# Performance work log

Measured on AMD Instinct MI355X. Metric: run time of the kernel, lower is better.

The kernel has to match this reference:

```python
import jax, jax.numpy as jnp
import numpy as np

WIN = 12     # SAMv3 window_size
HEADS = 8    # num_heads

def _window(t, win=WIN):
    B, H, W, C = t.shape
    t = t.reshape(B, H // win, win, W // win, win, C).transpose(0, 1, 3, 2, 4, 5)
    return t.reshape(B, (H // win) * (W // win), win * win, C)

def _unwindow(t, H, W, win=WIN):
    B, nW, S, C = t.shape
    t = t.reshape(B, H // win, W // win, win, win, C).transpose(0, 1, 3, 2, 4, 5)
    return t.reshape(B, H, W, C)

def _sam(fq, fkv, bias, wq, wk, wv, wo, bo):
    # Windowed, masked cross-frame multi-head attention (SAMv3).
    # fq, fkv: (B, C, H, W); bias: (B, nW, 1, 1, S) additive mask bias.
    B, C, H, W = fq.shape
    hd = C // HEADS
    scale = hd ** -0.5
    q = _window(jnp.einsum('bchw,cd->bhwd', fq, wq))   # (B,nW,S,C)
    k = _window(jnp.einsum('bchw,cd->bhwd', fkv, wk))
    v = _window(jnp.einsum('bchw,cd->bhwd', fkv, wv))
    nW, S = q.shape[1], q.shape[2]
    q = q.reshape(B, nW, S, HEADS, hd)
    k = k.reshape(B, nW, S, HEADS, hd)
    v = v.reshape(B, nW, S, HEADS, hd)
    attn = jnp.einsum('bnqhd,bnkhd->bnhqk', q, k) * scale + bias
    attn = jax.nn.softmax(attn, axis=-1)
    out = jnp.einsum('bnhqk,bnkhd->bnqhd', attn, v).reshape(B, nW, S, C)
    out = out @ wo + bo
    return _unwindow(out, H, W).transpose(0, 3, 1, 2)  # (B, C, H, W)

def setup_inputs() -> dict:
    key = jax.random.key(0)
    B, C, T, H, W = 2, 384, 2, 192, 192
    ks = jax.random.split(key, 16)
    d = {}
    d['x'] = jax.random.normal(ks[0], (B, C, T, H, W), jnp.float32)
    d['mask'] = jax.random.randint(ks[1], (B, T, 1, H, W), 0, 2, jnp.int32)
    names = ['sam1_wq', 'sam1_wk', 'sam1_wv', 'sam1_wo',
             'sam2_wq', 'sam2_wk', 'sam2_wv', 'sam2_wo',
             'proj1_w', 'proj2_w']
    for i, n in enumerate(names):
        d[n] = jax.random.normal(ks[2 + i], (C, C), jnp.float32) * 0.02
    d['sam1_bo'] = jnp.zeros((C,), jnp.float32)
    d['sam2_bo'] = jnp.zeros((C,), jnp.float32)
    d['proj1_b'] = jnp.zeros((C,), jnp.float32)
    d['proj2_b'] = jnp.zeros((C,), jnp.float32)
    return d

def reference(x, mask, sam1_wq, sam1_wk, sam1_wv, sam1_wo, sam1_bo,
              sam2_wq, sam2_wk, sam2_wv, sam2_wo, sam2_bo,
              proj1_w, proj1_b, proj2_w, proj2_b):
    # x: (B, C, T=2, H, W); mask: (B, T, 1, H, W)
    f1 = x[:, :, 0]
    f2 = x[:, :, 1]
    m = mask[:, 1, 0][..., None]                      # (B, H, W, 1), frame-2 mask
    mw = _window(m)[..., 0]                           # (B, nW, S)
    bias = jnp.where(mw == 0, -1e9, 0.0).astype(x.dtype)[:, :, None, None, :]
    o1 = _sam(f1, f2, bias, sam1_wq, sam1_wk, sam1_wv, sam1_wo, sam1_bo)
    x1 = jnp.einsum('bchw,dc->bdhw', o1, proj1_w) + proj1_b[None, :, None, None]
    o2 = _sam(f2, f1, bias, sam2_wq, sam2_wk, sam2_wv, sam2_wo, sam2_bo)
    x2 = jnp.einsum('bchw,dc->bdhw', o2, proj2_w) + proj2_b[None, :, None, None]
    return jnp.concatenate([x1[:, :, None], x2[:, :, None]], axis=2)  # (B, C, 2, H, W)
```

## Files before the change

kernel.cpp:

```cpp
#include <hip/hip_runtime.h>
#include <stdint.h>

typedef __attribute__((ext_vector_type(8))) short bf16x8;
typedef __attribute__((ext_vector_type(4))) float f32x4;

#define HW    36864
#define CCH   384
#define NPIX  73728
#define W2    147456

__device__ __forceinline__ unsigned short f2bf(float f) {
  unsigned u = __builtin_bit_cast(unsigned, f);
  u += 0x7FFFu + ((u >> 16) & 1u);
  return (unsigned short)(u >> 16);
}

typedef const unsigned int __attribute__((address_space(1)))* gas1_t;
typedef unsigned int __attribute__((address_space(3)))* las3_t;
__device__ __forceinline__ void gload16(const void* g, void* l) {
  __builtin_amdgcn_global_load_lds((gas1_t)g, (las3_t)l, 16, 0, 0);
}


__global__ void k_wt(const float* __restrict__ w0, const float* __restrict__ w1,
                     const float* __restrict__ w2, const float* __restrict__ w3,
                     const float* __restrict__ w4, const float* __restrict__ w5,
                     unsigned short* __restrict__ wt) {
  int idx = blockIdx.x * 256 + threadIdx.x;
  int w = blockIdx.y;
  const float* W;
  switch (w) { case 0: W = w0; break; case 1: W = w1; break;
               case 2: W = w2; break; case 3: W = w3; break;
               case 4: W = w4; break; default: W = w5; break; }
  const int slotmap[6] = {0, 4, 5, 3, 1, 2};
  int slot = slotmap[w];
  int c = idx / 384, d = idx % 384;
  wt[(size_t)slot * W2 + (size_t)d * 384 + c] = f2bf(W[(size_t)c * 384 + d]);
}

__global__ void k_wf(const float* __restrict__ wo1, const float* __restrict__ pj1,
                     const float* __restrict__ wo2, const float* __restrict__ pj2,
                     unsigned short* __restrict__ wfT) {
  int idx = blockIdx.x * 256 + threadIdx.x;
  int s = blockIdx.y;
  const float* wo = s ? wo2 : wo1;
  const float* pj = s ? pj2 : pj1;
  int d = idx / 384, e = idx % 384;
  float acc = 0.f;
  for (int c = 0; c < 384; ++c) acc += pj[d * 384 + c] * wo[e * 384 + c];
  wfT[(size_t)s * W2 + (size_t)d * 384 + e] = f2bf(acc);
}

__global__ void k_bf(const float* __restrict__ bo1, const float* __restrict__ pj1,
                     const float* __restrict__ pb1, const float* __restrict__ bo2,
                     const float* __restrict__ pj2, const float* __restrict__ pb2,
                     float* __restrict__ bfused) {
  int t = threadIdx.x;
  int s = t / 384, d = t % 384;
  const float* bo = s ? bo2 : bo1;
  const float* pj = s ? pj2 : pj1;
  const float* pb = s ? pb2 : pb1;
  float acc = pb[d];
  for (int c = 0; c < 384; ++c) acc += pj[d * 384 + c] * bo[c];
  bfused[t] = acc;
}

__global__ __launch_bounds__(256) void k_tx(const float* __restrict__ x,
                                            unsigned short* __restrict__ xbf) {
  __shared__ float tile[64][65];
  int p0 = blockIdx.x * 64;
  int c0 = blockIdx.y * 64;
  int bt = blockIdx.z;
  int b = bt >> 1, t = bt & 1;
  int tid = threadIdx.x;
  int cl = tid >> 2;
  int pq = (tid & 3) * 4;
  const float* src = x + (((size_t)b * CCH + (c0 + cl)) * 2 + t) * HW + p0;
#pragma unroll
  for (int i = 0; i < 4; ++i) {
    int p_l = pq + i * 16;
    float4 v = *reinterpret_cast<const float4*>(src + p_l);
    tile[cl][p_l + 0] = v.x; tile[cl][p_l + 1] = v.y;
    tile[cl][p_l + 2] = v.z; tile[cl][p_l + 3] = v.w;
  }
  __syncthreads();
  int pl = tid >> 2;
  int cq = (tid & 3) * 16;
  unsigned short* dst = xbf + ((size_t)(t * 2 + b) * HW + p0 + pl) * CCH + c0 + cq;
  bf16x8 o0, o1;
#pragma unroll
  for (int j = 0; j < 8; ++j) o0[j] = (short)f2bf(tile[cq + j][pl]);
#pragma unroll
  for (int j = 0; j < 8; ++j) o1[j] = (short)f2bf(tile[cq + 8 + j][pl]);
  *reinterpret_cast<bf16x8*>(dst) = o0;
  *reinterpret_cast<bf16x8*>(dst + 8) = o1;
}

template <int EPI>
__global__ __launch_bounds__(256) void gemm_bt(
    const unsigned short* __restrict__ A,
    const unsigned short* __restrict__ Bt,
    unsigned short* __restrict__ Cq,
    unsigned short* __restrict__ Ckv,
    int nsplit,
    float* __restrict__ Cf,
    const float* __restrict__ bias,
    int tsel, float oscale) {
  __shared__ __align__(16) unsigned short Lsh[3][8192];
  const int tid = threadIdx.x;
  const int lane = tid & 63;
  const int wid = tid >> 6, wr = wid >> 1, wc = wid & 1;

  const int gx = gridDim.x;
  const int nwg = gx * gridDim.y;
  const int bid = blockIdx.x + blockIdx.y * gx;
  const int chunk = nwg >> 3;
  const int l = (bid & 7) * chunk + (bid >> 3);
  const int bx = l % gx, by = l / gx;

  const int m0 = (EPI == 1 ? bx : by) * 128;
  const int n0 = (EPI == 1 ? by : bx) * 128;
  const int r15 = lane & 15, g = lane >> 4;

  const int u1 = tid + 256;
  const unsigned short* srcA0 = A + (size_t)(m0 + (tid >> 2)) * 384 + (((tid & 3) ^ ((tid >> 3) & 3)) << 3);
  const unsigned short* srcA1 = A + (size_t)(m0 + (u1 >> 2)) * 384 + (((u1 & 3) ^ ((u1 >> 3) & 3)) << 3);
  const unsigned short* srcB0 = Bt + (size_t)(n0 + (tid >> 2)) * 384 + (((tid & 3) ^ ((tid >> 3) & 3)) << 3);
  const unsigned short* srcB1 = Bt + (size_t)(n0 + (u1 >> 2)) * 384 + (((u1 & 3) ^ ((u1 >> 3) & 3)) << 3);
  const int wbase = (tid & ~63) * 8;

  f32x4 acc[4][4];
  f32x4 zero4 = {0.f, 0.f, 0.f, 0.f};
#pragma unroll
  for (int a = 0; a < 4; ++a)
#pragma unroll
    for (int b = 0; b < 4; ++b) acc[a][b] = zero4;

  const int swzr = (g ^ ((r15 >> 1) & 3)) << 3;

#define STAGE(buf, kt) do {                                  \
    int ke = (kt) * 32;                                      \
    gload16(srcA0 + ke, &Lsh[(buf)][wbase]);                 \
    gload16(srcA1 + ke, &Lsh[(buf)][2048 + wbase]);          \
    gload16(srcB0 + ke, &Lsh[(buf)][4096 + wbase]);          \
    gload16(srcB1 + ke, &Lsh[(buf)][6144 + wbase]);          \
  } while (0)

#define COMPUTE(buf) do {                                                       \
    bf16x8 af[4], bfv[4];                                                       \
    _Pragma("unroll")                                                           \
    for (int a = 0; a < 4; ++a)                                                 \
      af[a] = *(const bf16x8*)&Lsh[(buf)][(wr * 64 + a * 16 + r15) * 32 + swzr];\
    _Pragma("unroll")                                                           \
    for (int b = 0; b < 4; ++b)                                                 \
      bfv[b] = *(const bf16x8*)&Lsh[(buf)][4096 + (wc * 64 + b * 16 + r15) * 32 + swzr];\
    _Pragma("unroll")                                                           \
    for (int a = 0; a < 4; ++a)                                                 \
      _Pragma("unroll")                                                         \
      for (int b = 0; b < 4; ++b)                                               \
        acc[a][b] = __builtin_amdgcn_mfma_f32_16x16x32_bf16(af[a], bfv[b], acc[a][b], 0, 0, 0);\
  } while (0)

  STAGE(0, 0);
  STAGE(1, 1);
#pragma unroll
  for (int kt = 0; kt < 11; ++kt) {
    asm volatile("s_waitcnt vmcnt(4)" ::: "memory");
    __builtin_amdgcn_s_barrier();
    asm volatile("" ::: "memory");
    if (kt < 10) STAGE((kt + 2) % 3, kt + 2);
    COMPUTE(kt % 3);
  }
  __syncthreads();
  COMPUTE(11 % 3);
#undef STAGE
#undef COMPUTE

  if (EPI == 2) {
    unsigned short* Cp;
    int ldc2, ncol0;
    float sc;
    if (n0 < nsplit) { Cp = Cq;  ldc2 = 384; ncol0 = n0;          sc = oscale; }
    else             { Cp = Ckv; ldc2 = 768; ncol0 = n0 - nsplit; sc = 1.0f;   }
#pragma unroll
    for (int a = 0; a < 4; ++a) {
      size_t rbase = (size_t)(m0 + wr * 64 + a * 16 + g * 4) * ldc2;
#pragma unroll
      for (int b = 0; b < 4; ++b) {
        int n = ncol0 + wc * 64 + b * 16 + r15;
        unsigned short* cp = Cp + rbase + n;
#pragma unroll
        for (int r = 0; r < 4; ++r) cp[(size_t)r * ldc2] = f2bf(acc[a][b][r] * sc);
      }
    }
  } else {
    int bb = n0 / HW;
#pragma unroll
    for (int a = 0; a < 4; ++a) {
      int d = m0 + wr * 64 + a * 16 + g * 4;
#pragma unroll
      for (int b = 0; b < 4; ++b) {
        int n = n0 + wc * 64 + b * 16 + r15;
        int p = n - bb * HW;
#pragma unroll
        for (int r = 0; r < 4; ++r) {
          float v = acc[a][b][r] + bias[d + r];
          Cf[(((size_t)bb * CCH + (d + r)) * 2 + tsel) * HW + p] = v;
        }
      }
    }
  }
}

__global__ __launch_bounds__(512, 2) void attn_kernel(
    const unsigned short* __restrict__ q,
    const unsigned short* __restrict__ kv,
    const int* __restrict__ mask,
    unsigned short* __restrict__ obuf) {
  __shared__ __align__(16) unsigned short P[8][16][168];
  __shared__ int ptab[144];
  const int n = blockIdx.x, b = blockIdx.y;
  const int tid = threadIdx.x;
  const int h = tid >> 6, lane = tid & 63;
  const int c15 = lane & 15, g = lane >> 4;
  const int wy = n >> 4, wx = n & 15;
  const size_t rowbase = (size_t)b * HW;
  const int* mrow = mask + (size_t)(b * 2 + 1) * HW;

  if (tid < 144)
    ptab[tid] = (wy * 12 + tid / 12) * 192 + wx * 12 + tid % 12;

  for (int idx = lane; idx < 16 * 24; idx += 64)
    P[h][idx / 24][144 + (idx % 24)] = 0;
  __syncthreads();

  float biasv[9];
#pragma unroll
  for (int nt = 0; nt < 9; ++nt)
    biasv[nt] = (mrow[ptab[nt * 16 + c15]] == 0) ? -1e9f : 0.0f;

  bf16x8 zfrag = {0, 0, 0, 0, 0, 0, 0, 0};
  f32x4 zero4 = {0.f, 0.f, 0.f, 0.f};

  bf16x8 kf0[9], kf1[9];
#pragma unroll
  for (int nt = 0; nt < 9; ++nt) {
    const unsigned short* kp = kv + (rowbase + ptab[nt * 16 + c15]) * 768 + h * 48;
    kf0[nt] = *(const bf16x8*)(kp + g * 8);
    kf1[nt] = zfrag;
    if (g < 2) kf1[nt] = *(const bf16x8*)(kp + 32 + g * 8);
  }

  const unsigned short* vb = kv + rowbase * 768 + 384 + h * 48;
  bf16x8 vf[5][3];
#pragma unroll
  for (int ks = 0; ks < 5; ++ks) {
#pragma unroll
    for (int dt = 0; dt < 3; ++dt) {
      bf16x8 v = {0, 0, 0, 0, 0, 0, 0, 0};
#pragma unroll
      for (int j = 0; j < 8; ++j) {
        int sk = ks * 32 + g * 8 + j;
        if (sk < 144)
          v[j] = (short)vb[(size_t)ptab[sk] * 768 + dt * 16 + c15];
      }
      vf[ks][dt] = v;
    }
  }

  bf16x8 qf0, qf1;
  {
    const unsigned short* qp = q + (rowbase + ptab[c15]) * 384 + h * 48;
    qf0 = *(const bf16x8*)(qp + g * 8);
    qf1 = zfrag;
    if (g < 2) qf1 = *(const bf16x8*)(qp + 32 + g * 8);
  }

  for (int mt = 0; mt < 9; ++mt) {
    bf16x8 qn0 = zfrag, qn1 = zfrag;
    if (mt < 8) {
      const unsigned short* qp = q + (rowbase + ptab[(mt + 1) * 16 + c15]) * 384 + h * 48;
      qn0 = *(const bf16x8*)(qp + g * 8);
      if (g < 2) qn1 = *(const bf16x8*)(qp + 32 + g * 8);
    }

    float l4[4] = {0.f, 0.f, 0.f, 0.f};
    f32x4 oacc[3];
#pragma unroll
    for (int dt = 0; dt < 3; ++dt) oacc[dt] = zero4;

#pragma unroll
    for (int nt = 0; nt < 9; ++nt) {
      f32x4 s = __builtin_amdgcn_mfma_f32_16x16x32_bf16(qf1, kf1[nt], zero4, 0, 0, 0);
      s = __builtin_amdgcn_mfma_f32_16x16x32_bf16(qf0, kf0[nt], s, 0, 0, 0);
#pragma unroll
      for (int r = 0; r < 4; ++r) {
        float pv = __expf(s[r] + biasv[nt]);
        l4[r] += pv;
        P[h][g * 4 + r][nt * 16 + c15] = f2bf(pv);
      }
      if (nt & 1) {
        int ks = nt >> 1;
        bf16x8 pf = *(const bf16x8*)&P[h][c15][ks * 32 + g * 8];
#pragma unroll
        for (int dt = 0; dt < 3; ++dt)
          oacc[dt] = __builtin_amdgcn_mfma_f32_16x16x32_bf16(pf, vf[ks][dt], oacc[dt], 0, 0, 0);
      }
    }
    {
      bf16x8 pf = *(const bf16x8*)&P[h][c15][4 * 32 + g * 8];
#pragma unroll
      for (int dt = 0; dt < 3; ++dt)
        oacc[dt] = __builtin_amdgcn_mfma_f32_16x16x32_bf16(pf, vf[4][dt], oacc[dt], 0, 0, 0);
    }

#pragma unroll
    for (int s = 1; s < 16; s <<= 1)
#pragma unroll
      for (int r = 0; r < 4; ++r) l4[r] += __shfl_xor(l4[r], s, 64);

    float inv[4];
#pragma unroll
    for (int r = 0; r < 4; ++r) inv[r] = 1.0f / l4[r];
#pragma unroll
    for (int dt = 0; dt < 3; ++dt) {
#pragma unroll
      for (int r = 0; r < 4; ++r) {
        int so = mt * 16 + g * 4 + r;
        obuf[(rowbase + ptab[so]) * 384 + h * 48 + dt * 16 + c15] =
            f2bf(oacc[dt][r] * inv[r]);
      }
    }

    qf0 = qn0; qf1 = qn1;
  }
}

extern "C" void kernel_launch(void* const* d_in, const int* in_sizes, int n_in,
                              void* d_out, int out_size, void* d_ws, size_t ws_size,
                              hipStream_t stream) {
  const float* x    = (const float*)d_in[0];
  const int*   mask = (const int*)d_in[1];
  const float* wq1 = (const float*)d_in[2];
  const float* wk1 = (const float*)d_in[3];
  const float* wv1 = (const float*)d_in[4];
  const float* wo1 = (const float*)d_in[5];
  const float* wq2 = (const float*)d_in[6];
  const float* wk2 = (const float*)d_in[7];
  const float* wv2 = (const float*)d_in[8];
  const float* wo2 = (const float*)d_in[9];
  const float* pj1 = (const float*)d_in[10];
  const float* pj2 = (const float*)d_in[11];
  const float* bo1 = (const float*)d_in[12];
  const float* bo2 = (const float*)d_in[13];
  const float* pb1 = (const float*)d_in[14];
  const float* pb2 = (const float*)d_in[15];
  float* out = (float*)d_out;

  const float SCALE = 0.14433756729740643f;

  char* ws = (char*)d_ws;
  size_t off = 0;
  unsigned short* wt   = (unsigned short*)(ws + off); off += (size_t)6 * W2 * 2;
  unsigned short* wfT  = (unsigned short*)(ws + off); off += (size_t)2 * W2 * 2;
  float*          bfu  = (float*)(ws + off);          off += (size_t)2 * 384 * 4;
  unsigned short* xbf  = (unsigned short*)(ws + off); off += (size_t)4 * HW * CCH * 2;
  size_t fixed = off;

  size_t qsz = (size_t)NPIX * 384 * 2, kvsz = (size_t)NPIX * 768 * 2, osz = qsz;
  bool fused = (ws_size >= fixed + 2 * qsz + 2 * kvsz + osz);
  if (!fused && ws_size < fixed + qsz + kvsz + osz) return;

  k_wt<<<dim3(576, 6), 256, 0, stream>>>(wq1, wk1, wv1, wq2, wk2, wv2, wt);
  k_wf<<<dim3(576, 2), 256, 0, stream>>>(wo1, pj1, wo2, pj2, wfT);
  k_bf<<<1, 768, 0, stream>>>(bo1, pj1, pb1, bo2, pj2, pb2, bfu);
  k_tx<<<dim3(576, 6, 4), 256, 0, stream>>>(x, xbf);

  if (fused) {
    unsigned short* qb[2] = {(unsigned short*)(ws + fixed),
                             (unsigned short*)(ws + fixed + qsz)};
    unsigned short* kvb[2] = {(unsigned short*)(ws + fixed + 2 * qsz),
                              (unsigned short*)(ws + fixed + 2 * qsz + kvsz)};
    unsigned short* obuf = (unsigned short*)(ws + fixed + 2 * qsz + 2 * kvsz);
    for (int f = 0; f < 2; ++f) {
      gemm_bt<2><<<dim3(9, 576), 256, 0, stream>>>(
          xbf + (size_t)f * 2 * HW * CCH, wt + (size_t)f * 3 * W2,
          qb[f], kvb[1 - f], 384, nullptr, nullptr, 0, SCALE);
    }
    for (int s = 0; s < 2; ++s) {
      attn_kernel<<<dim3(256, 2), 512, 0, stream>>>(qb[s], kvb[s], mask, obuf);
      gemm_bt<1><<<dim3(3, 576), 256, 0, stream>>>(
          wfT + (size_t)s * W2, obuf, nullptr, nullptr, 0, out, bfu + s * 384, s, 1.0f);
    }
  } else {
    unsigned short* qbuf = (unsigned short*)(ws + fixed);
    unsigned short* kvbuf = (unsigned short*)(ws + fixed + qsz);
    unsigned short* obuf = (unsigned short*)(ws + fixed + qsz + kvsz);
    for (int s = 0; s < 2; ++s) {
      const unsigned short* fq = xbf + (size_t)(s == 0 ? 0 : 1) * 2 * HW * CCH;
      const unsigned short* fk = xbf + (size_t)(s == 0 ? 1 : 0) * 2 * HW * CCH;
      gemm_bt<2><<<dim3(3, 576), 256, 0, stream>>>(
          fq, wt + (size_t)(s == 0 ? 0 : 3) * W2, qbuf, nullptr, 384,
          nullptr, nullptr, 0, SCALE);
      gemm_bt<2><<<dim3(6, 576), 256, 0, stream>>>(
          fk, wt + (size_t)(s == 0 ? 4 : 1) * W2, nullptr, kvbuf, 0,
          nullptr, nullptr, 0, 1.0f);
      attn_kernel<<<dim3(256, 2), 512, 0, stream>>>(qbuf, kvbuf, mask, obuf);
      gemm_bt<1><<<dim3(3, 576), 256, 0, stream>>>(
          wfT + (size_t)s * W2, obuf, nullptr, nullptr, 0, out, bfu + s * 384, s, 1.0f);
    }
  }
}
```

Measured before the change: 678.4 us.

## Fuse output projection GEMM into attention kernel epilogue

The attention kernel now writes each window's normalized output into a padded LDS tile instead of a global bf16 buffer. After a block barrier, every head-wave multiplies that tile by its 48-row slice of the fused output/projection weight with MFMA, adds the fused bias, and stores fp32 results straight into the final output layout. This drops the intermediate obuf round trip, two GEMM launches and the non-fused workspace fallback path. In exchange the attention block uses about 160KB of LDS, which likely cuts residency to one block per CU despite the two-block launch bound. It also holds many weight fragments in registers and makes uncoalesced window-scattered fp32 stores.

```diff
diff --git a/kernel.cpp b/kernel.cpp
--- a/kernel.cpp
+++ b/kernel.cpp
@@ -96,16 +96,12 @@
   *reinterpret_cast<bf16x8*>(dst + 8) = o1;
 }
 
-template <int EPI>
-__global__ __launch_bounds__(256) void gemm_bt(
+__global__ __launch_bounds__(256) void gemm_qkv(
     const unsigned short* __restrict__ A,
     const unsigned short* __restrict__ Bt,
     unsigned short* __restrict__ Cq,
     unsigned short* __restrict__ Ckv,
-    int nsplit,
-    float* __restrict__ Cf,
-    const float* __restrict__ bias,
-    int tsel, float oscale) {
+    float oscale) {
   __shared__ __align__(16) unsigned short Lsh[3][8192];
   const int tid = threadIdx.x;
   const int lane = tid & 63;
@@ -118,8 +114,8 @@
   const int l = (bid & 7) * chunk + (bid >> 3);
   const int bx = l % gx, by = l / gx;
 
-  const int m0 = (EPI == 1 ? bx : by) * 128;
-  const int n0 = (EPI == 1 ? by : bx) * 128;
+  const int m0 = by * 128;
+  const int n0 = bx * 128;
   const int r15 = lane & 15, g = lane >> 4;
 
   const int u1 = tid + 256;
@@ -176,48 +172,35 @@
 #undef STAGE
 #undef COMPUTE
 
-  if (EPI == 2) {
-    unsigned short* Cp;
-    int ldc2, ncol0;
-    float sc;
-    if (n0 < nsplit) { Cp = Cq;  ldc2 = 384; ncol0 = n0;          sc = oscale; }
-    else             { Cp = Ckv; ldc2 = 768; ncol0 = n0 - nsplit; sc = 1.0f;   }
-#pragma unroll
-    for (int a = 0; a < 4; ++a) {
-      size_t rbase = (size_t)(m0 + wr * 64 + a * 16 + g * 4) * ldc2;
-#pragma unroll
-      for (int b = 0; b < 4; ++b) {
-        int n = ncol0 + wc * 64 + b * 16 + r15;
-        unsigned short* cp = Cp + rbase + n;
-#pragma unroll
-        for (int r = 0; r < 4; ++r) cp[(size_t)r * ldc2] = f2bf(acc[a][b][r] * sc);
-      }
-    }
-  } else {
-    int bb = n0 / HW;
-#pragma unroll
-    for (int a = 0; a < 4; ++a) {
-      int d = m0 + wr * 64 + a * 16 + g * 4;
-#pragma unroll
-      for (int b = 0; b < 4; ++b) {
-        int n = n0 + wc * 64 + b * 16 + r15;
-        int p = n - bb * HW;
-#pragma unroll
-        for (int r = 0; r < 4; ++r) {
-          float v = acc[a][b][r] + bias[d + r];
-          Cf[(((size_t)bb * CCH + (d + r)) * 2 + tsel) * HW + p] = v;
-        }
-      }
-    }
-  }
-}
-
+  unsigned short* Cp;
+  int ldc2, ncol0;
+  float sc;
+  if (n0 < 384) { Cp = Cq;  ldc2 = 384; ncol0 = n0;       sc = oscale; }
+  else          { Cp = Ckv; ldc2 = 768; ncol0 = n0 - 384; sc = 1.0f;   }
+#pragma unroll
+  for (int a = 0; a < 4; ++a) {
+    size_t rbase = (size_t)(m0 + wr * 64 + a * 16 + g * 4) * ldc2;
+#pragma unroll
+    for (int b = 0; b < 4; ++b) {
+      int n = ncol0 + wc * 64 + b * 16 + r15;
+      unsigned short* cp = Cp + rbase + n;
+#pragma unroll
+      for (int r = 0; r < 4; ++r) cp[(size_t)r * ldc2] = f2bf(acc[a][b][r] * sc);
+    }
+  }
+}
+
+#define OPAD 408
 __global__ __launch_bounds__(512, 2) void attn_kernel(
     const unsigned short* __restrict__ q,
     const unsigned short* __restrict__ kv,
     const int* __restrict__ mask,
-    unsigned short* __restrict__ obuf) {
+    const unsigned short* __restrict__ wfT,
+    const float* __restrict__ bfu,
+    float* __restrict__ out,
+    int tsel) {
   __shared__ __align__(16) unsigned short P[8][16][168];
+  __shared__ __align__(16) unsigned short O_lds[144 * OPAD];
   __shared__ int ptab[144];
   const int n = blockIdx.x, b = blockIdx.y;
   const int tid = threadIdx.x;
@@ -327,12 +310,51 @@
 #pragma unroll
       for (int r = 0; r < 4; ++r) {
         int so = mt * 16 + g * 4 + r;
-        obuf[(rowbase + ptab[so]) * 384 + h * 48 + dt * 16 + c15] =
-            f2bf(oacc[dt][r] * inv[r]);
+        O_lds[so * OPAD + h * 48 + dt * 16 + c15] = f2bf(oacc[dt][r] * inv[r]);
       }
     }
 
     qf0 = qn0; qf1 = qn1;
+  }
+
+  __syncthreads();
+
+  {
+    const unsigned short* wrow = wfT + (size_t)(h * 48) * 384;
+    bf16x8 af[3][12];
+#pragma unroll
+    for (int mt2 = 0; mt2 < 3; ++mt2)
+#pragma unroll
+      for (int kt = 0; kt < 12; ++kt)
+        af[mt2][kt] = *(const bf16x8*)(wrow + (size_t)(mt2 * 16 + c15) * 384 + kt * 32 + g * 8);
+
+    float bias12[3][4];
+#pragma unroll
+    for (int mt2 = 0; mt2 < 3; ++mt2)
+#pragma unroll
+      for (int r = 0; r < 4; ++r)
+        bias12[mt2][r] = bfu[h * 48 + mt2 * 16 + g * 4 + r];
+
+#pragma unroll
+    for (int ct = 0; ct < 9; ++ct) {
+      bf16x8 bfr[12];
+#pragma unroll
+      for (int kt = 0; kt < 12; ++kt)
+        bfr[kt] = *(const bf16x8*)&O_lds[(ct * 16 + c15) * OPAD + kt * 32 + g * 8];
+      int pcol = ptab[ct * 16 + c15];
+#pragma unroll
+      for (int mt2 = 0; mt2 < 3; ++mt2) {
+        f32x4 acc = zero4;
+#pragma unroll
+        for (int kt = 0; kt < 12; ++kt)
+          acc = __builtin_amdgcn_mfma_f32_16x16x32_bf16(af[mt2][kt], bfr[kt], acc, 0, 0, 0);
+#pragma unroll
+        for (int r = 0; r < 4; ++r) {
+          int d = h * 48 + mt2 * 16 + g * 4 + r;
+          out[((size_t)(b * CCH + d) * 2 + tsel) * HW + pcol] = acc[r] + bias12[mt2][r];
+        }
+      }
+    }
   }
 }
 
@@ -365,49 +387,27 @@
   unsigned short* wfT  = (unsigned short*)(ws + off); off += (size_t)2 * W2 * 2;
   float*          bfu  = (float*)(ws + off);          off += (size_t)2 * 384 * 4;
   unsigned short* xbf  = (unsigned short*)(ws + off); off += (size_t)4 * HW * CCH * 2;
-  size_t fixed = off;
-
-  size_t qsz = (size_t)NPIX * 384 * 2, kvsz = (size_t)NPIX * 768 * 2, osz = qsz;
-  bool fused = (ws_size >= fixed + 2 * qsz + 2 * kvsz + osz);
-  if (!fused && ws_size < fixed + qsz + kvsz + osz) return;
+  size_t qsz = (size_t)NPIX * 384 * 2, kvsz = (size_t)NPIX * 768 * 2;
+  unsigned short* qb0  = (unsigned short*)(ws + off); off += qsz;
+  unsigned short* qb1  = (unsigned short*)(ws + off); off += qsz;
+  unsigned short* kvb0 = (unsigned short*)(ws + off); off += kvsz;
+  unsigned short* kvb1 = (unsigned short*)(ws + off); off += kvsz;
+  if (ws_size < off) return;
+  unsigned short* qb[2]  = {qb0, qb1};
+  unsigned short* kvb[2] = {kvb0, kvb1};
 
   k_wt<<<dim3(576, 6), 256, 0, stream>>>(wq1, wk1, wv1, wq2, wk2, wv2, wt);
   k_wf<<<dim3(576, 2), 256, 0, stream>>>(wo1, pj1, wo2, pj2, wfT);
   k_bf<<<1, 768, 0, stream>>>(bo1, pj1, pb1, bo2, pj2, pb2, bfu);
   k_tx<<<dim3(576, 6, 4), 256, 0, stream>>>(x, xbf);
 
-  if (fused) {
-    unsigned short* qb[2] = {(unsigned short*)(ws + fixed),
-                             (unsigned short*)(ws + fixed + qsz)};
-    unsigned short* kvb[2] = {(unsigned short*)(ws + fixed + 2 * qsz),
-                              (unsigned short*)(ws + fixed + 2 * qsz + kvsz)};
-    unsigned short* obuf = (unsigned short*)(ws + fixed + 2 * qsz + 2 * kvsz);
-    for (int f = 0; f < 2; ++f) {
-      gemm_bt<2><<<dim3(9, 576), 256, 0, stream>>>(
-          xbf + (size_t)f * 2 * HW * CCH, wt + (size_t)f * 3 * W2,
-          qb[f], kvb[1 - f], 384, nullptr, nullptr, 0, SCALE);
-    }
-    for (int s = 0; s < 2; ++s) {
-      attn_kernel<<<dim3(256, 2), 512, 0, stream>>>(qb[s], kvb[s], mask, obuf);
-      gemm_bt<1><<<dim3(3, 576), 256, 0, stream>>>(
-          wfT + (size_t)s * W2, obuf, nullptr, nullptr, 0, out, bfu + s * 384, s, 1.0f);
-    }
-  } else {
-    unsigned short* qbuf = (unsigned short*)(ws + fixed);
-    unsigned short* kvbuf = (unsigned short*)(ws + fixed + qsz);
-    unsigned short* obuf = (unsigned short*)(ws + fixed + qsz + kvsz);
-    for (int s = 0; s < 2; ++s) {
-      const unsigned short* fq = xbf + (size_t)(s == 0 ? 0 : 1) * 2 * HW * CCH;
-      const unsigned short* fk = xbf + (size_t)(s == 0 ? 1 : 0) * 2 * HW * CCH;
-      gemm_bt<2><<<dim3(3, 576), 256, 0, stream>>>(
-          fq, wt + (size_t)(s == 0 ? 0 : 3) * W2, qbuf, nullptr, 384,
-          nullptr, nullptr, 0, SCALE);
-      gemm_bt<2><<<dim3(6, 576), 256, 0, stream>>>(
-          fk, wt + (size_t)(s == 0 ? 4 : 1) * W2, nullptr, kvbuf, 0,
-          nullptr, nullptr, 0, 1.0f);
-      attn_kernel<<<dim3(256, 2), 512, 0, stream>>>(qbuf, kvbuf, mask, obuf);
-      gemm_bt<1><<<dim3(3, 576), 256, 0, stream>>>(
-          wfT + (size_t)s * W2, obuf, nullptr, nullptr, 0, out, bfu + s * 384, s, 1.0f);
-    }
-  }
-}
+  for (int f = 0; f < 2; ++f) {
+    gemm_qkv<<<dim3(9, 576), 256, 0, stream>>>(
+        xbf + (size_t)f * 2 * HW * CCH, wt + (size_t)f * 3 * W2,
+        qb[f], kvb[1 - f], SCALE);
+  }
+  for (int s = 0; s < 2; ++s) {
+    attn_kernel<<<dim3(256, 2), 512, 0, stream>>>(
+        qb[s], kvb[s], mask, wfT + (size_t)s * W2, bfu + s * 384, out, s);
+  }
+}
```

After: 743.6 us. 1.1x slower.
